# Kernel tuning notes

Measured on AMD Instinct MI355X. Metric: run time of the kernel, lower is better.

## Reference

```python
import jax, jax.numpy as jnp
import numpy as np
from jax import lax

SIZE = 4      # pool stride / patch stride
PAD = 1       # patch halo -> window = SIZE + 2*PAD = 6
K1 = 5        # mask mixing kernel
TOPK = 240    # hard-coded number of refinement regions per batch element


def conv2d(x, w, b, pad):
    # x: [B,Cin,H,W], w: [Cout,Cin,kh,kw] (torch OIHW layout)
    y = lax.conv_general_dilated(x, w, (1, 1), [(pad, pad), (pad, pad)],
                                 dimension_numbers=("NCHW", "OIHW", "NCHW"))
    return y + b[None, :, None, None]


def setup_inputs() -> dict:
    key = jax.random.key(0)
    ks = jax.random.split(key, 7)
    B, C, H, W = 16, 50, 256, 256
    out_lr = jax.random.normal(ks[0], (B, C, H, W), dtype=jnp.float32)
    s = 0.05  # keep conv outputs / softmax numerics sane
    return {
        "out_lr": out_lr,
        "W1": jax.random.normal(ks[1], (C, C, 3, 3), jnp.float32) * s,
        "b1": jax.random.normal(ks[2], (C,), jnp.float32) * s,
        "W2": jax.random.normal(ks[3], (2, C, 3, 3), jnp.float32) * s,
        "b2": jax.random.normal(ks[4], (2,), jnp.float32) * s,
        "Wk": jax.random.normal(ks[5], (K1 * K1, 1, 1, 1), jnp.float32) * s,
        "bk": jax.random.normal(ks[6], (K1 * K1,), jnp.float32) * s,
    }


def reference(out_lr, W1, b1, W2, b2, Wk, bk):
    B, C, H, W = out_lr.shape
    Hs, Ws = H // SIZE, W // SIZE

    # spa_mask_1 Sequential: conv3x3 -> ReLU -> conv3x3 (nf -> 2 channels)
    x = jax.nn.relu(conv2d(out_lr, W1, b1, 1))
    x = conv2d(x, W2, b2, 1)                      # [B,2,H,W]

    # softmax_t over channel dim (t=1), keep channel 1
    sm = jax.nn.softmax(x, axis=1)[:, 1:2]        # [B,1,H,W]

    # adaptive_avg_pool2d to (H/4, W/4) == 4x4 avg pool (H,W divisible by SIZE)
    sm = sm.reshape(B, 1, Hs, SIZE, Ws, SIZE).mean(axis=(3, 5))  # [B,1,Hs,Ws]
    sm = jnp.where(sm >= 0, sm, 0.1 * sm)         # LeakyReLU(0.1)

    # 1x1 conv producing per-position 5x5 mixing kernel
    kern = conv2d(sm, Wk, bk, 0)[:, None]         # [B,1,25,Hs,Ws]

    # F.unfold(pad=2, kernel 5x5): 25 sliding windows in row-major (ki,kj) order
    p = (K1 - 1) // 2
    smp = jnp.pad(sm, ((0, 0), (0, 0), (p, p), (p, p)))
    windows = jnp.stack([smp[:, :, i:i + Hs, j:j + Ws]
                         for i in range(K1) for j in range(K1)], axis=2)  # [B,1,25,Hs,Ws]

    final_mask = (kern * windows).sum(axis=2)     # [B,1,Hs,Ws]

    # topk 240 per batch; scatter->nonzero in torch yields row-major sorted flat indices
    err = final_mask.reshape(B, Hs * Ws)
    _, idx = lax.top_k(err, TOPK)                 # [B,240]
    idx = jnp.sort(idx, axis=1)
    b_idx = jnp.repeat(jnp.arange(B), TOPK)       # [B*240]
    flat = idx.reshape(-1)
    h_idx = flat // Ws
    w_idx = flat % Ws

    # crop_patch: pad by 1, gather 6x6 patches at stride 4 (direct gather, no full unfold)
    padded = jnp.pad(out_lr, ((0, 0), (0, 0), (PAD, PAD), (PAD, PAD)))
    win = SIZE + 2 * PAD

    def get_patch(b, h, w):
        return lax.dynamic_slice(padded, (b, 0, h * SIZE, w * SIZE), (1, C, win, win))[0]

    patches = jax.vmap(get_patch)(b_idx, h_idx, w_idx)  # [B*240, C, 6, 6]
    return patches, b_idx, h_idx, w_idx, final_mask
```

## Files before the change

kernel.cpp:

```cpp
#include <hip/hip_runtime.h>
#include <math.h>

#define CCH   50
#define HH    256
#define WW    256
#define BATCH 16
#define HSZ   64
#define WSZ   64
#define NTOP  240
#define SPX   66
#define SROW  6

typedef __attribute__((ext_vector_type(8))) short s16x8;
typedef __attribute__((ext_vector_type(4))) float f32x4;

__device__ __forceinline__ unsigned short bf16rne(float x) {
  unsigned u = __float_as_uint(x);
  unsigned r = (u + 0x7FFFu + ((u >> 16) & 1u)) >> 16;
  return (unsigned short)r;
}
__device__ __forceinline__ float bf2f(unsigned short h) {
  return __uint_as_float(((unsigned)h) << 16);
}

__global__ __launch_bounds__(64) void prep_wfrag_k(
    const float* __restrict__ W1, unsigned short* __restrict__ wf) {
  int combo = blockIdx.x;
  int lane = threadIdx.x;
  int sp = combo & 1;
  int t2 = combo >> 1;
  int mt = t2 & 3;
  int t3 = t2 >> 2;
  int tap = t3 % 9;
  int chunk = t3 / 9;
  int co = mt * 16 + (lane & 15);
  int gbase = combo * 512 + lane * 8;
#pragma unroll
  for (int e = 0; e < 8; ++e) {
    int ci = chunk * 32 + ((lane >> 4) * 8) + e;
    float w = (co < CCH && ci < CCH) ? W1[co * (CCH * 9) + ci * 9 + tap] : 0.f;
    unsigned short h = bf16rne(w);
    unsigned short v = sp ? bf16rne(w - bf2f(h)) : h;
    wf[gbase + e] = v;
  }
}

__global__ __launch_bounds__(256, 3) void conv1_mfma_k(
    const float* __restrict__ in, const unsigned short* __restrict__ wf,
    const float* __restrict__ b1, float* __restrict__ x1p) {
  __shared__ alignas(16) short xlds[SROW * SPX * 64];

  int bx = blockIdx.x;
  int pq = bx & 3;
  int rg = (bx >> 2) & 63;
  int b  = bx >> 8;
  int row0 = rg * 4;
  int px0g = pq * 64;

  int t = threadIdx.x;
  int lane = t & 63;
  int wv = t >> 6;
  int ln15 = lane & 15;
  int lg = lane >> 4;

  f32x4 acc[4][4];
#pragma unroll
  for (int mt = 0; mt < 4; ++mt)
#pragma unroll
    for (int s = 0; s < 4; ++s) acc[mt][s] = (f32x4){0.f, 0.f, 0.f, 0.f};

  const size_t in_b = ((size_t)b * CCH) << 16;

#pragma unroll
  for (int chunk = 0; chunk < 2; ++chunk) {
    __syncthreads();
    for (int i = t; i < SROW * 4 * SPX; i += 256) {
      int ro = i / SPX;
      int px = i - ro * SPX;
      int row = ro >> 2, oct = ro & 3;
      int gr = row0 - 1 + row;
      int gx = px0g - 1 + px;
      bool okxy = (gr >= 0 && gr < HH && gx >= 0 && gx < WW);
      const float* gp = in + in_b + ((size_t)(chunk * 32 + oct * 8) << 16)
                        + (gr << 8) + gx;
      unsigned hs[8], ls[8];
#pragma unroll
      for (int e = 0; e < 8; ++e) {
        int ci = chunk * 32 + oct * 8 + e;
        float x = (okxy && ci < CCH) ? gp[(size_t)e << 16] : 0.f;
        unsigned u = __float_as_uint(x);
        unsigned hu = u & 0xFFFF0000u;
        float lo = x - __uint_as_float(hu);
        unsigned ul = __float_as_uint(lo);
        hs[e] = hu >> 16;
        ls[e] = (ul + 0x7FFFu + ((ul >> 16) & 1u)) >> 16;
      }
      s16x8 hv, lv;
#pragma unroll
      for (int e = 0; e < 8; ++e) { hv[e] = (short)hs[e]; lv[e] = (short)ls[e]; }
      int swz = (px & 7) << 3;
      int base_sh = (row * SPX + px) * 64;
      *(s16x8*)&xlds[base_sh + ((oct * 8) ^ swz)] = hv;
      *(s16x8*)&xlds[base_sh + ((32 + oct * 8) ^ swz)] = lv;
    }
    __syncthreads();

#pragma unroll
    for (int tap = 0; tap < 9; ++tap) {
      const int dh = tap / 3 - 1;
      const int dw = tap % 3 - 1;
      s16x8 ah[4], al[4];
#pragma unroll
      for (int mt = 0; mt < 4; ++mt) {
        int cb = ((chunk * 9 + tap) * 4 + mt) * 2;
        ah[mt] = *(const s16x8*)(wf + (size_t)cb * 512 + lane * 8);
        al[mt] = *(const s16x8*)(wf + (size_t)(cb + 1) * 512 + lane * 8);
      }
      int rbase = (wv + 1 + dh) * (SPX * 64);
#pragma unroll
      for (int s = 0; s < 4; ++s) {
        int pixL = 1 + s * 16 + ln15 + dw;
        int bsh = rbase + pixL * 64;
        int swz = (pixL & 7) << 3;
        s16x8 bh = *(const s16x8*)&xlds[bsh + ((lg * 8) ^ swz)];
        s16x8 bl = *(const s16x8*)&xlds[bsh + ((32 + lg * 8) ^ swz)];
#pragma unroll
        for (int mt = 0; mt < 4; ++mt) {
          acc[mt][s] = __builtin_amdgcn_mfma_f32_16x16x32_bf16(
              ah[mt], bh, acc[mt][s], 0, 0, 0);
          acc[mt][s] = __builtin_amdgcn_mfma_f32_16x16x32_bf16(
              ah[mt], bl, acc[mt][s], 0, 0, 0);
          acc[mt][s] = __builtin_amdgcn_mfma_f32_16x16x32_bf16(
              al[mt], bh, acc[mt][s], 0, 0, 0);
        }
      }
    }
  }

  int orow = row0 + wv;
#pragma unroll
  for (int s = 0; s < 4; ++s) {
    int px = px0g + s * 16 + ln15;
#pragma unroll
    for (int mt = 0; mt < 4; ++mt) {
#pragma unroll
      for (int reg = 0; reg < 4; ++reg) {
        int co = mt * 16 + lg * 4 + reg;
        if (co < CCH) {
          float v = fmaxf(acc[mt][s][reg] + b1[co], 0.f);
          x1p[(((size_t)b * CCH + co) << 16) + (orow << 8) + px] = v;
        }
      }
    }
  }
}

__global__ __launch_bounds__(256) void conv2_softmax_k(
    const float* __restrict__ x1p, const float* __restrict__ w2,
    const float* __restrict__ b2, float* __restrict__ sm) {
  int pb = blockIdx.x;
  int l = (pb & 7) * 128 + (pb >> 3);
  int b  = l >> 6;
  int rg = l & 63;
  int row0 = rg * 4;
  int px = threadIdx.x;

  float a0, a1, a2, a3, c0, c1, c2, c3;
  a0 = a1 = a2 = a3 = b2[0];
  c0 = c1 = c2 = c3 = b2[1];
  bool wm = px > 0, wp = px < WW - 1;

  const float* xb = x1p + (((size_t)b * CCH) << 16);

#define TAP(T, A, C) { \
    A = fmaf(wc0[3 * (T)], lf, A); A = fmaf(wc0[3 * (T) + 1], m, A); \
    A = fmaf(wc0[3 * (T) + 2], rt, A); \
    C = fmaf(wc1[3 * (T)], lf, C); C = fmaf(wc1[3 * (T) + 1], m, C); \
    C = fmaf(wc1[3 * (T) + 2], rt, C); }

#define ROW(IR, BODY) { \
    int gr = row0 - 1 + (IR); \
    if (gr >= 0 && gr < HH) { \
      const float* rp = xp + (gr << 8); \
      float m  = rp[px]; \
      float lf = wm ? rp[px - 1] : 0.f; \
      float rt = wp ? rp[px + 1] : 0.f; \
      BODY \
    } }

  for (int ci = 0; ci < CCH; ++ci) {
    const float* xp = xb + ((size_t)ci << 16);
    const float* wc0 = w2 + ci * 9;
    const float* wc1 = w2 + 450 + ci * 9;
    ROW(0, TAP(0, a0, c0))
    ROW(1, TAP(0, a1, c1) TAP(1, a0, c0))
    ROW(2, TAP(0, a2, c2) TAP(1, a1, c1) TAP(2, a0, c0))
    ROW(3, TAP(0, a3, c3) TAP(1, a2, c2) TAP(2, a1, c1))
    ROW(4, TAP(1, a3, c3) TAP(2, a2, c2))
    ROW(5, TAP(2, a3, c3))
  }
#undef ROW
#undef TAP

  size_t so = ((size_t)b << 16) + (row0 << 8) + px;
  sm[so]       = 1.f / (1.f + expf(a0 - c0));
  sm[so + 256] = 1.f / (1.f + expf(a1 - c1));
  sm[so + 512] = 1.f / (1.f + expf(a2 - c2));
  sm[so + 768] = 1.f / (1.f + expf(a3 - c3));
}

__global__ __launch_bounds__(256) void pool_leaky_k(
    const float* __restrict__ sm, float* __restrict__ pool) {
  int idx = blockIdx.x * 256 + threadIdx.x;
  int b = idx >> 12, hw = idx & 4095;
  int hs = hw >> 6, ws = hw & 63;
  const float* p = sm + (size_t)b * 65536 + hs * 4 * WW + ws * 4;
  float s = 0.f;
#pragma unroll
  for (int r = 0; r < 4; ++r)
#pragma unroll
    for (int c = 0; c < 4; ++c) s += p[r * WW + c];
  s *= (1.f / 16.f);
  pool[idx] = (s >= 0.f) ? s : 0.1f * s;
}

__global__ __launch_bounds__(256) void mix_mask_k(
    const float* __restrict__ pool, const float* __restrict__ wk,
    const float* __restrict__ bk, float* __restrict__ mask_out) {
  int idx = blockIdx.x * 256 + threadIdx.x;
  int b = idx >> 12, hw = idx & 4095;
  int hs = hw >> 6, ws = hw & 63;
  float c = pool[idx];
  float s = 0.f;
#pragma unroll
  for (int i = 0; i < 5; ++i) {
#pragma unroll
    for (int j = 0; j < 5; ++j) {
      int y = hs + i - 2, x = ws + j - 2;
      float win = (y >= 0 && y < HSZ && x >= 0 && x < WSZ)
                      ? pool[(size_t)b * 4096 + y * WSZ + x] : 0.f;
      int k = i * 5 + j;
      s += (wk[k] * c + bk[k]) * win;
    }
  }
  mask_out[idx] = s;
}

__global__ __launch_bounds__(256) void topk_sort_k(
    const float* __restrict__ mask, float* __restrict__ ob, float* __restrict__ oh,
    float* __restrict__ ow, int* __restrict__ idx_ws) {
  __shared__ unsigned long long keys[4096];
  __shared__ int sidx[256];
  int b = blockIdx.x, t = threadIdx.x;

  for (int i = t; i < 4096; i += 256) {
    float v = mask[(size_t)b * 4096 + i];
    unsigned u = __float_as_uint(v);
    u = (u & 0x80000000u) ? ~u : (u | 0x80000000u);
    u = ~u;
    keys[i] = ((unsigned long long)u << 12) | (unsigned)i;
  }
  __syncthreads();

  for (int k = 2; k <= 4096; k <<= 1) {
    for (int j = k >> 1; j > 0; j >>= 1) {
      for (int m = t; m < 2048; m += 256) {
        int i = ((m & ~(j - 1)) << 1) | (m & (j - 1));
        int l = i | j;
        bool up = ((i & k) == 0);
        unsigned long long a = keys[i], c = keys[l];
        if ((a > c) == up) { keys[i] = c; keys[l] = a; }
      }
      __syncthreads();
    }
  }

  sidx[t] = (t < NTOP) ? (int)(keys[t] & 0xFFFu) : 0x7FFFFFFF;
  __syncthreads();
  for (int k = 2; k <= 256; k <<= 1) {
    for (int j = k >> 1; j > 0; j >>= 1) {
      if (t < 128) {
        int i = ((t & ~(j - 1)) << 1) | (t & (j - 1));
        int l = i | j;
        bool up = ((i & k) == 0);
        int a = sidx[i], c = sidx[l];
        if ((a > c) == up) { sidx[i] = c; sidx[l] = a; }
      }
      __syncthreads();
    }
  }

  if (t < NTOP) {
    int id = sidx[t];
    int o = b * NTOP + t;
    ob[o] = (float)b;
    oh[o] = (float)(id >> 6);
    ow[o] = (float)(id & 63);
    idx_ws[o] = id;
  }
}

__global__ __launch_bounds__(256) void gather_patch_k(
    const float* __restrict__ in, const int* __restrict__ idx_ws,
    float* __restrict__ patches) {
  int p = blockIdx.x;
  int b = p / NTOP;
  int id = idx_ws[p];
  int h = id >> 6, w = id & 63;
  int y0 = h * 4 - 1, x0 = w * 4 - 1;
  const float* base = in + (size_t)b * CCH * 65536;
  float* op = patches + (size_t)p * (CCH * 36);
  for (int e = threadIdx.x; e < CCH * 36; e += 256) {
    int c = e / 36;
    int r = (e - c * 36) / 6;
    int col = e - c * 36 - r * 6;
    int y = y0 + r, x = x0 + col;
    float v = 0.f;
    if (y >= 0 && y < HH && x >= 0 && x < WW)
      v = base[(size_t)c * 65536 + y * WW + x];
    op[e] = v;
  }
}

extern "C" void kernel_launch(void* const* d_in, const int* in_sizes, int n_in,
                              void* d_out, int out_size, void* d_ws, size_t ws_size,
                              hipStream_t stream) {
  const float* out_lr = (const float*)d_in[0];
  const float* W1 = (const float*)d_in[1];
  const float* b1 = (const float*)d_in[2];
  const float* W2 = (const float*)d_in[3];
  const float* b2 = (const float*)d_in[4];
  const float* Wk = (const float*)d_in[5];
  const float* bk = (const float*)d_in[6];

  float* x1p  = (float*)d_ws;
  float* sm   = x1p + (size_t)52428800;
  float* pool = sm + (size_t)1048576;
  int*  idxb  = (int*)(pool + 65536);
  unsigned short* wfrag = (unsigned short*)(pool + 65536 + 3840);

  float* out    = (float*)d_out;
  float* o_patch = out;
  float* o_b    = out + (size_t)6912000;
  float* o_h    = o_b + 3840;
  float* o_w    = o_h + 3840;
  float* o_mask = o_w + 3840;

  prep_wfrag_k<<<144, 64, 0, stream>>>(W1, wfrag);
  conv1_mfma_k<<<BATCH * 64 * 4, 256, 0, stream>>>(out_lr, wfrag, b1, x1p);
  conv2_softmax_k<<<BATCH * 64, 256, 0, stream>>>(x1p, W2, b2, sm);
  pool_leaky_k<<<256, 256, 0, stream>>>(sm, pool);
  mix_mask_k<<<256, 256, 0, stream>>>(pool, Wk, bk, o_mask);
  topk_sort_k<<<BATCH, 256, 0, stream>>>(o_mask, o_b, o_h, o_w, idxb);
  gather_patch_k<<<BATCH * NTOP, 256, 0, stream>>>(out_lr, idxb, o_patch);
}
```

Before: 434.8 us.

## Fuse softmax-pool into conv2, merge mask mixing with top-k, raise MFMA priority

The 4x4 average pool and LeakyReLU move into the conv2 epilogue: per-column sums are reduced across four lanes with shuffles, so the full-resolution softmax map is no longer written and read back. The 5x5 mask mixing is folded into the top-k kernel, which now runs 1024 threads per batch element, cutting two kernel launches and one round trip through global memory. The MFMA block in conv1 is also bracketed with s_setprio so matrix instructions get scheduling priority. The top-k step still uses only 16 blocks, and the larger block size may add cost in the sort phases.

```diff
diff --git a/kernel.cpp b/kernel.cpp
--- a/kernel.cpp
+++ b/kernel.cpp
@@ -124,6 +124,7 @@
         int swz = (pixL & 7) << 3;
         s16x8 bh = *(const s16x8*)&xlds[bsh + ((lg * 8) ^ swz)];
         s16x8 bl = *(const s16x8*)&xlds[bsh + ((32 + lg * 8) ^ swz)];
+        __builtin_amdgcn_s_setprio(1);
 #pragma unroll
         for (int mt = 0; mt < 4; ++mt) {
           acc[mt][s] = __builtin_amdgcn_mfma_f32_16x16x32_bf16(
@@ -133,6 +134,7 @@
           acc[mt][s] = __builtin_amdgcn_mfma_f32_16x16x32_bf16(
               al[mt], bh, acc[mt][s], 0, 0, 0);
         }
+        __builtin_amdgcn_s_setprio(0);
       }
     }
   }
@@ -155,9 +157,9 @@
   }
 }
 
-__global__ __launch_bounds__(256) void conv2_softmax_k(
+__global__ __launch_bounds__(256) void conv2_pool_k(
     const float* __restrict__ x1p, const float* __restrict__ w2,
-    const float* __restrict__ b2, float* __restrict__ sm) {
+    const float* __restrict__ b2, float* __restrict__ pool) {
   int pb = blockIdx.x;
   int l = (pb & 7) * 128 + (pb >> 3);
   int b  = l >> 6;
@@ -202,60 +204,43 @@
 #undef ROW
 #undef TAP
 
-  size_t so = ((size_t)b << 16) + (row0 << 8) + px;
-  sm[so]       = 1.f / (1.f + expf(a0 - c0));
-  sm[so + 256] = 1.f / (1.f + expf(a1 - c1));
-  sm[so + 512] = 1.f / (1.f + expf(a2 - c2));
-  sm[so + 768] = 1.f / (1.f + expf(a3 - c3));
-}
-
-__global__ __launch_bounds__(256) void pool_leaky_k(
-    const float* __restrict__ sm, float* __restrict__ pool) {
-  int idx = blockIdx.x * 256 + threadIdx.x;
-  int b = idx >> 12, hw = idx & 4095;
-  int hs = hw >> 6, ws = hw & 63;
-  const float* p = sm + (size_t)b * 65536 + hs * 4 * WW + ws * 4;
-  float s = 0.f;
-#pragma unroll
-  for (int r = 0; r < 4; ++r)
-#pragma unroll
-    for (int c = 0; c < 4; ++c) s += p[r * WW + c];
-  s *= (1.f / 16.f);
-  pool[idx] = (s >= 0.f) ? s : 0.1f * s;
-}
-
-__global__ __launch_bounds__(256) void mix_mask_k(
+  float s = 1.f / (1.f + expf(a0 - c0)) + 1.f / (1.f + expf(a1 - c1))
+          + 1.f / (1.f + expf(a2 - c2)) + 1.f / (1.f + expf(a3 - c3));
+  s += __shfl_xor(s, 1);
+  s += __shfl_xor(s, 2);
+  if ((px & 3) == 0) {
+    float p = s * (1.f / 16.f);
+    pool[(size_t)b * 4096 + rg * 64 + (px >> 2)] = (p >= 0.f) ? p : 0.1f * p;
+  }
+}
+
+__global__ __launch_bounds__(1024) void mixtopk_k(
     const float* __restrict__ pool, const float* __restrict__ wk,
-    const float* __restrict__ bk, float* __restrict__ mask_out) {
-  int idx = blockIdx.x * 256 + threadIdx.x;
-  int b = idx >> 12, hw = idx & 4095;
-  int hs = hw >> 6, ws = hw & 63;
-  float c = pool[idx];
-  float s = 0.f;
-#pragma unroll
-  for (int i = 0; i < 5; ++i) {
-#pragma unroll
-    for (int j = 0; j < 5; ++j) {
-      int y = hs + i - 2, x = ws + j - 2;
-      float win = (y >= 0 && y < HSZ && x >= 0 && x < WSZ)
-                      ? pool[(size_t)b * 4096 + y * WSZ + x] : 0.f;
-      int k = i * 5 + j;
-      s += (wk[k] * c + bk[k]) * win;
-    }
-  }
-  mask_out[idx] = s;
-}
-
-__global__ __launch_bounds__(256) void topk_sort_k(
-    const float* __restrict__ mask, float* __restrict__ ob, float* __restrict__ oh,
-    float* __restrict__ ow, int* __restrict__ idx_ws) {
+    const float* __restrict__ bk, float* __restrict__ mask_out,
+    float* __restrict__ ob, float* __restrict__ oh, float* __restrict__ ow,
+    int* __restrict__ idx_ws) {
   __shared__ unsigned long long keys[4096];
   __shared__ int sidx[256];
   int b = blockIdx.x, t = threadIdx.x;
 
-  for (int i = t; i < 4096; i += 256) {
-    float v = mask[(size_t)b * 4096 + i];
-    unsigned u = __float_as_uint(v);
+  const float* pb = pool + (size_t)b * 4096;
+  for (int i = t; i < 4096; i += 1024) {
+    int hs = i >> 6, ws = i & 63;
+    float c = pb[i];
+    float s = 0.f;
+#pragma unroll
+    for (int ki = 0; ki < 5; ++ki) {
+#pragma unroll
+      for (int kj = 0; kj < 5; ++kj) {
+        int y = hs + ki - 2, x = ws + kj - 2;
+        float win = (y >= 0 && y < HSZ && x >= 0 && x < WSZ)
+                        ? pb[y * WSZ + x] : 0.f;
+        int k = ki * 5 + kj;
+        s += (wk[k] * c + bk[k]) * win;
+      }
+    }
+    mask_out[(size_t)b * 4096 + i] = s;
+    unsigned u = __float_as_uint(s);
     u = (u & 0x80000000u) ? ~u : (u | 0x80000000u);
     u = ~u;
     keys[i] = ((unsigned long long)u << 12) | (unsigned)i;
@@ -264,7 +249,7 @@
 
   for (int k = 2; k <= 4096; k <<= 1) {
     for (int j = k >> 1; j > 0; j >>= 1) {
-      for (int m = t; m < 2048; m += 256) {
+      for (int m = t; m < 2048; m += 1024) {
         int i = ((m & ~(j - 1)) << 1) | (m & (j - 1));
         int l = i | j;
         bool up = ((i & k) == 0);
@@ -275,7 +260,7 @@
     }
   }
 
-  sidx[t] = (t < NTOP) ? (int)(keys[t] & 0xFFFu) : 0x7FFFFFFF;
+  if (t < 256) sidx[t] = (t < NTOP) ? (int)(keys[t] & 0xFFFu) : 0x7FFFFFFF;
   __syncthreads();
   for (int k = 2; k <= 256; k <<= 1) {
     for (int j = k >> 1; j > 0; j >>= 1) {
@@ -334,8 +319,7 @@
   const float* bk = (const float*)d_in[6];
 
   float* x1p  = (float*)d_ws;
-  float* sm   = x1p + (size_t)52428800;
-  float* pool = sm + (size_t)1048576;
+  float* pool = x1p + (size_t)52428800;
   int*  idxb  = (int*)(pool + 65536);
   unsigned short* wfrag = (unsigned short*)(pool + 65536 + 3840);
 
@@ -348,9 +332,7 @@
 
   prep_wfrag_k<<<144, 64, 0, stream>>>(W1, wfrag);
   conv1_mfma_k<<<BATCH * 64 * 4, 256, 0, stream>>>(out_lr, wfrag, b1, x1p);
-  conv2_softmax_k<<<BATCH * 64, 256, 0, stream>>>(x1p, W2, b2, sm);
-  pool_leaky_k<<<256, 256, 0, stream>>>(sm, pool);
-  mix_mask_k<<<256, 256, 0, stream>>>(pool, Wk, bk, o_mask);
-  topk_sort_k<<<BATCH, 256, 0, stream>>>(o_mask, o_b, o_h, o_w, idxb);
+  conv2_pool_k<<<BATCH * 64, 256, 0, stream>>>(x1p, W2, b2, pool);
+  mixtopk_k<<<BATCH, 1024, 0, stream>>>(pool, Wk, bk, o_mask, o_b, o_h, o_w, idxb);
   gather_patch_k<<<BATCH * NTOP, 256, 0, stream>>>(out_lr, idxb, o_patch);
 }
```

After: 389.9 us (median of 2 runs). -10.3%, faster.
